# Kernel tuning notes

Measured on AMD Instinct MI355X. Metric: run time of the kernel, lower is better.

## Reference

```python
import jax, jax.numpy as jnp
import numpy as np

B, N, D = 8, 2048, 512   # batch, ctx_size, input_size
P, H = 16, 32            # num_pers, hidden_size


def setup_inputs() -> dict:
    key = jax.random.key(0)
    k1, k2 = jax.random.split(key)
    context = jax.random.normal(k1, (B, N, D), dtype=jnp.float32)
    # stacked weights of the 16 bias-free nn.Linear(input_size, hidden_size) layers
    # xavier-uniform-style scale: sqrt(6/(fan_in+fan_out))
    limit = np.sqrt(6.0 / (D + H)).astype(np.float32)
    W = jax.random.uniform(k2, (P, H, D), dtype=jnp.float32, minval=-limit, maxval=limit)
    ctx_mask = jnp.ones((B, N), dtype=jnp.int32)
    return {"context": context, "W": W, "ctx_mask": ctx_mask}


def reference(context, W, ctx_mask):
    # per-persona projection + relu: [P, B, N, H]
    fc = jax.nn.relu(jnp.einsum('bnd,phd->pbnh', context, W))
    # sum over personas of fc @ fc^T, then average: [B, N, N]
    att = jnp.einsum('pbnh,pbmh->bnm', fc, fc) / P
    # NOTE: original uses F.softmax(attention, dim=1) -> softmax over rows (axis=1)
    att = jax.nn.softmax(att, axis=1)
    # masked_fill with markoff_value=0 on masked columns then masked rows
    m = ctx_mask.astype(att.dtype)          # [B, N]
    att = att * m[:, None, :] * m[:, :, None]
    return att
```

## Files before the change

### kernel.cpp

```cpp
#include <hip/hip_runtime.h>

#define Bc 8
#define Nc 2048
#define Dc 512
#define PH 512
#define NN 4194304
#define NT 136

#define BM 128
#define BN 128
#define BK 32

typedef __attribute__((ext_vector_type(8))) short bf16x8;
typedef __attribute__((ext_vector_type(4))) float f32x4;

static __device__ __forceinline__ unsigned short f2b(float x) {
    union { float f; unsigned u; } v; v.f = x;
    unsigned r = v.u + 0x7fffu + ((v.u >> 16) & 1u);
    return (unsigned short)(r >> 16);
}

static __device__ __forceinline__ void load16_lds(const unsigned short* g, unsigned short* l) {
    __builtin_amdgcn_global_load_lds(
        (const __attribute__((address_space(1))) void*)g,
        (__attribute__((address_space(3))) void*)l,
        16, 0, 0);
}

__global__ __launch_bounds__(256) void prep_kernel(
    const float* __restrict__ ctx, const float* __restrict__ W,
    unsigned short* __restrict__ Xb, unsigned short* __restrict__ Wb,
    float* __restrict__ rsum) {
    int t = blockIdx.x * 256 + threadIdx.x;
    if (t < 2097152) {
        float4 v = ((const float4*)ctx)[t];
        ushort4 o;
        o.x = f2b(v.x); o.y = f2b(v.y); o.z = f2b(v.z); o.w = f2b(v.w);
        ((ushort4*)Xb)[t] = o;
    }
    if (t < 65536) {
        float4 v = ((const float4*)W)[t];
        ushort4 o;
        o.x = f2b(v.x); o.y = f2b(v.y); o.z = f2b(v.z); o.w = f2b(v.w);
        ((ushort4*)Wb)[t] = o;
    }
    if (t < 4096) {
        float4 z; z.x = 0.f; z.y = 0.f; z.z = 0.f; z.w = 0.f;
        ((float4*)rsum)[t] = z;
    }
}

__global__ __launch_bounds__(256) void gemm1_relu(
    const unsigned short* __restrict__ Xb, const unsigned short* __restrict__ Wb,
    unsigned short* __restrict__ F) {
    __shared__ unsigned short As[BM * BK];
    __shared__ unsigned short Bs[BN * BK];
    const int tid = threadIdx.x;
    const int lane = tid & 63;
    const int wave = tid >> 6;
    const int wm = wave >> 1, wn = wave & 1;
    const int row0 = blockIdx.y * BM;
    const int col0 = blockIdx.x * BN;

    f32x4 acc[4][4] = {};

    for (int k0 = 0; k0 < Dc; k0 += BK) {
#pragma unroll
        for (int j = 0; j < 2; ++j) {
            int e = j * 256 + tid;
            int rr = e >> 2, cc = e & 3;
            load16_lds(&Xb[(size_t)(row0 + rr) * Dc + k0 + cc * 8], &As[e * 8]);
            load16_lds(&Wb[(size_t)(col0 + rr) * Dc + k0 + cc * 8], &Bs[e * 8]);
        }
        __syncthreads();

        bf16x8 af[4], bfr[4];
#pragma unroll
        for (int i = 0; i < 4; ++i) {
            af[i]  = *(const bf16x8*)&As[(wm * 64 + i * 16 + (lane & 15)) * BK + (lane >> 4) * 8];
            bfr[i] = *(const bf16x8*)&Bs[(wn * 64 + i * 16 + (lane & 15)) * BK + (lane >> 4) * 8];
        }
#pragma unroll
        for (int mi = 0; mi < 4; ++mi)
#pragma unroll
            for (int ni = 0; ni < 4; ++ni)
                acc[mi][ni] = __builtin_amdgcn_mfma_f32_16x16x32_bf16(af[mi], bfr[ni], acc[mi][ni], 0, 0, 0);
        __syncthreads();
    }

#pragma unroll
    for (int mi = 0; mi < 4; ++mi) {
#pragma unroll
        for (int ni = 0; ni < 4; ++ni) {
            int col  = col0 + wn * 64 + ni * 16 + (lane & 15);
            int rowb = row0 + wm * 64 + mi * 16 + ((lane >> 4) << 2);
#pragma unroll
            for (int r = 0; r < 4; ++r) {
                float v = fmaxf(acc[mi][ni][r], 0.0f);
                F[(size_t)(rowb + r) * PH + col] = f2b(v);
            }
        }
    }
}

__global__ __launch_bounds__(256) void gemm2_store(
    const unsigned short* __restrict__ F, float* __restrict__ rsum,
    float* __restrict__ Ework) {
    __shared__ unsigned short As[BM * BK];
    __shared__ unsigned short Bs[BN * BK];
    const int tid = threadIdx.x;
    const int lane = tid & 63;
    const int wave = tid >> 6;
    const int wm = wave >> 1, wn = wave & 1;
    const int l15 = lane & 15, q = lane >> 4;
    const int b = blockIdx.x & 7;
    const int idx = blockIdx.x >> 3;

    int j = 0;
    while (((j + 1) * (j + 2) / 2) <= idx) ++j;
    int i = idx - j * (j + 1) / 2;
    const int row0 = i * BM;
    const int col0 = j * BN;
    const unsigned short* Fb = F + (size_t)b * Nc * PH;

    f32x4 acc[4][4] = {};

    for (int k0 = 0; k0 < PH; k0 += BK) {
#pragma unroll
        for (int jj = 0; jj < 2; ++jj) {
            int e = jj * 256 + tid;
            int rr = e >> 2, cc = e & 3;
            load16_lds(&Fb[(size_t)(row0 + rr) * PH + k0 + cc * 8], &As[e * 8]);
            load16_lds(&Fb[(size_t)(col0 + rr) * PH + k0 + cc * 8], &Bs[e * 8]);
        }
        __syncthreads();

        bf16x8 af[4], bfr[4];
#pragma unroll
        for (int qq = 0; qq < 4; ++qq) {
            af[qq]  = *(const bf16x8*)&As[(wm * 64 + qq * 16 + l15) * BK + q * 8];
            bfr[qq] = *(const bf16x8*)&Bs[(wn * 64 + qq * 16 + l15) * BK + q * 8];
        }
#pragma unroll
        for (int mi = 0; mi < 4; ++mi)
#pragma unroll
            for (int ni = 0; ni < 4; ++ni)
                acc[mi][ni] = __builtin_amdgcn_mfma_f32_16x16x32_bf16(af[mi], bfr[ni], acc[mi][ni], 0, 0, 0);
        __syncthreads();
    }

    float* Et = Ework + (size_t)(b * NT + idx) * 16384;

    float csum[4] = {0.f, 0.f, 0.f, 0.f};
    float rsm[4][4];
#pragma unroll
    for (int mi = 0; mi < 4; ++mi)
#pragma unroll
        for (int r = 0; r < 4; ++r) rsm[mi][r] = 0.f;

#pragma unroll
    for (int mi = 0; mi < 4; ++mi) {
#pragma unroll
        for (int ni = 0; ni < 4; ++ni) {
#pragma unroll
            for (int r = 0; r < 4; ++r) {
                float e = __expf(acc[mi][ni][r] * 0.0625f - 32.0f);
                Et[(wm * 64 + mi * 16 + (q << 2) + r) * 128 + wn * 64 + ni * 16 + l15] = e;
                csum[ni] += e;
                rsm[mi][r] += e;
            }
        }
    }
#pragma unroll
    for (int ni = 0; ni < 4; ++ni) {
        float s = csum[ni];
        s += __shfl_xor(s, 16);
        s += __shfl_xor(s, 32);
        if ((lane >> 4) == 0)
            atomicAdd(&rsum[b * Nc + col0 + wn * 64 + ni * 16 + lane], s);
    }
    if (i != j) {
#pragma unroll
        for (int mi = 0; mi < 4; ++mi) {
#pragma unroll
            for (int r = 0; r < 4; ++r) {
                float s = rsm[mi][r];
                s += __shfl_xor(s, 1);
                s += __shfl_xor(s, 2);
                s += __shfl_xor(s, 4);
                s += __shfl_xor(s, 8);
                if ((lane & 15) == 0)
                    atomicAdd(&rsum[b * Nc + row0 + wm * 64 + mi * 16 + ((lane >> 4) << 2) + r], s);
            }
        }
    }
}

__global__ __launch_bounds__(256) void invr_kernel(
    const float* __restrict__ rsum, const int* __restrict__ mask,
    float* __restrict__ invr) {
    int t = blockIdx.x * 256 + threadIdx.x;
    if (t < Bc * Nc) invr[t] = (float)mask[t] / rsum[t];
}

__global__ __launch_bounds__(256) void scatter_out(
    const float* __restrict__ Ework, const float* __restrict__ invr,
    const int* __restrict__ mask, float* __restrict__ out) {
    __shared__ float Ts[32 * 132];
    const int tid = threadIdx.x;
    const int b = blockIdx.x & 7;
    const int idx = blockIdx.x >> 3;

    int j = 0;
    while (((j + 1) * (j + 2) / 2) <= idx) ++j;
    int i = idx - j * (j + 1) / 2;
    const int row0 = i * BM;
    const int col0 = j * BN;

    const float* Et   = Ework + (size_t)(b * NT + idx) * 16384;
    const float* invb = invr + b * Nc;
    const int*   mb   = mask + b * Nc;
    float* outb = out + (size_t)b * NN;

    const int cl = tid >> 3, f0 = tid & 7;
    const int mc = tid >> 1, h  = tid & 1;

    for (int ci = 0; ci < 4; ++ci) {
        if (ci) __syncthreads();
        const int r = ci * 32 + cl;
        const int n = row0 + r;
        const float mrow = (float)mb[n];
#pragma unroll
        for (int g = 0; g < 4; ++g) {
            int f = f0 + 8 * g;
            float4 ev = *(const float4*)&Et[r * 128 + 4 * f];
            *(float4*)&Ts[cl * 132 + 4 * f] = ev;
            float4 iv = *(const float4*)&invb[col0 + 4 * f];
            float4 o;
            o.x = ev.x * iv.x * mrow;
            o.y = ev.y * iv.y * mrow;
            o.z = ev.z * iv.z * mrow;
            o.w = ev.w * iv.w * mrow;
            *(float4*)&outb[(size_t)n * Nc + col0 + 4 * f] = o;
        }
        if (i == j) continue;
        __syncthreads();
        const int a = col0 + mc;
        const float mcol = (float)mb[a];
        const int nb0 = row0 + ci * 32 + 16 * h;
#pragma unroll
        for (int u = 0; u < 4; ++u) {
            float4 iv = *(const float4*)&invb[nb0 + 4 * u];
            float4 o;
            o.x = Ts[(16 * h + 4 * u + 0) * 132 + mc] * iv.x * mcol;
            o.y = Ts[(16 * h + 4 * u + 1) * 132 + mc] * iv.y * mcol;
            o.z = Ts[(16 * h + 4 * u + 2) * 132 + mc] * iv.z * mcol;
            o.w = Ts[(16 * h + 4 * u + 3) * 132 + mc] * iv.w * mcol;
            *(float4*)&outb[(size_t)a * Nc + nb0 + 4 * u] = o;
        }
    }
}

__global__ __launch_bounds__(256) void gemm2_rsum(
    const unsigned short* __restrict__ F, float* __restrict__ rsum) {
    __shared__ unsigned short As[BM * BK];
    __shared__ unsigned short Bs[BN * BK];
    const int tid = threadIdx.x;
    const int lane = tid & 63;
    const int wave = tid >> 6;
    const int wm = wave >> 1, wn = wave & 1;
    const int b = blockIdx.y;

    int idx = blockIdx.x;
    int j = 0;
    while (((j + 1) * (j + 2) / 2) <= idx) ++j;
    int i = idx - j * (j + 1) / 2;
    const int row0 = i * BM;
    const int col0 = j * BN;
    const unsigned short* Fb = F + (size_t)b * Nc * PH;

    f32x4 acc[4][4] = {};

    for (int k0 = 0; k0 < PH; k0 += BK) {
#pragma unroll
        for (int jj = 0; jj < 2; ++jj) {
            int e = jj * 256 + tid;
            int rr = e >> 2, cc = e & 3;
            load16_lds(&Fb[(size_t)(row0 + rr) * PH + k0 + cc * 8], &As[e * 8]);
            load16_lds(&Fb[(size_t)(col0 + rr) * PH + k0 + cc * 8], &Bs[e * 8]);
        }
        __syncthreads();

        bf16x8 af[4], bfr[4];
#pragma unroll
        for (int q = 0; q < 4; ++q) {
            af[q]  = *(const bf16x8*)&As[(wm * 64 + q * 16 + (lane & 15)) * BK + (lane >> 4) * 8];
            bfr[q] = *(const bf16x8*)&Bs[(wn * 64 + q * 16 + (lane & 15)) * BK + (lane >> 4) * 8];
        }
#pragma unroll
        for (int mi = 0; mi < 4; ++mi)
#pragma unroll
            for (int ni = 0; ni < 4; ++ni)
                acc[mi][ni] = __builtin_amdgcn_mfma_f32_16x16x32_bf16(af[mi], bfr[ni], acc[mi][ni], 0, 0, 0);
        __syncthreads();
    }

    float csum[4] = {0.f, 0.f, 0.f, 0.f};
    float rsm[4][4];
#pragma unroll
    for (int mi = 0; mi < 4; ++mi)
#pragma unroll
        for (int r = 0; r < 4; ++r) rsm[mi][r] = 0.f;

#pragma unroll
    for (int mi = 0; mi < 4; ++mi) {
#pragma unroll
        for (int ni = 0; ni < 4; ++ni) {
#pragma unroll
            for (int r = 0; r < 4; ++r) {
                float e = __expf(acc[mi][ni][r] * 0.0625f - 32.0f);
                csum[ni] += e;
                rsm[mi][r] += e;
            }
        }
    }
#pragma unroll
    for (int ni = 0; ni < 4; ++ni) {
        float s = csum[ni];
        s += __shfl_xor(s, 16);
        s += __shfl_xor(s, 32);
        if ((lane >> 4) == 0)
            atomicAdd(&rsum[b * Nc + col0 + wn * 64 + ni * 16 + lane], s);
    }
    if (i != j) {
#pragma unroll
        for (int mi = 0; mi < 4; ++mi) {
#pragma unroll
            for (int r = 0; r < 4; ++r) {
                float s = rsm[mi][r];
                s += __shfl_xor(s, 1);
                s += __shfl_xor(s, 2);
                s += __shfl_xor(s, 4);
                s += __shfl_xor(s, 8);
                if ((lane & 15) == 0)
                    atomicAdd(&rsum[b * Nc + row0 + wm * 64 + mi * 16 + ((lane >> 4) << 2) + r], s);
            }
        }
    }
}

__global__ __launch_bounds__(256) void gemm2_write_sym(
    const unsigned short* __restrict__ F, const float* __restrict__ invr,
    const int* __restrict__ mask, float* __restrict__ out) {
    __shared__ unsigned short As[BM * BK];
    __shared__ unsigned short Bs[BN * BK];
    __shared__ float Ts[32 * 132];
    const int tid = threadIdx.x;
    const int lane = tid & 63;
    const int wave = tid >> 6;
    const int wm = wave >> 1, wn = wave & 1;
    const int l15 = lane & 15, q = lane >> 4;
    const int b = blockIdx.y;

    int idx = blockIdx.x;
    int j = 0;
    while (((j + 1) * (j + 2) / 2) <= idx) ++j;
    int i = idx - j * (j + 1) / 2;
    const int row0 = i * BM;
    const int col0 = j * BN;
    const unsigned short* Fb = F + (size_t)b * Nc * PH;

    f32x4 acc[4][4] = {};

    for (int k0 = 0; k0 < PH; k0 += BK) {
#pragma unroll
        for (int jj = 0; jj < 2; ++jj) {
            int e = jj * 256 + tid;
            int rr = e >> 2, cc = e & 3;
            load16_lds(&Fb[(size_t)(row0 + rr) * PH + k0 + cc * 8], &As[e * 8]);
            load16_lds(&Fb[(size_t)(col0 + rr) * PH + k0 + cc * 8], &Bs[e * 8]);
        }
        __syncthreads();

        bf16x8 af[4], bfr[4];
#pragma unroll
        for (int qq = 0; qq < 4; ++qq) {
            af[qq]  = *(const bf16x8*)&As[(wm * 64 + qq * 16 + l15) * BK + q * 8];
            bfr[qq] = *(const bf16x8*)&Bs[(wn * 64 + qq * 16 + l15) * BK + q * 8];
        }
#pragma unroll
        for (int mi = 0; mi < 4; ++mi)
#pragma unroll
            for (int ni = 0; ni < 4; ++ni)
                acc[mi][ni] = __builtin_amdgcn_mfma_f32_16x16x32_bf16(af[mi], bfr[ni], acc[mi][ni], 0, 0, 0);
        __syncthreads();
    }

#pragma unroll
    for (int mi = 0; mi < 4; ++mi)
#pragma unroll
        for (int ni = 0; ni < 4; ++ni)
#pragma unroll
            for (int r = 0; r < 4; ++r)
                acc[mi][ni][r] = __expf(acc[mi][ni][r] * 0.0625f - 32.0f);

    float* outb = out + (size_t)b * NN;

    float iv[4];
#pragma unroll
    for (int ni = 0; ni < 4; ++ni)
        iv[ni] = invr[b * Nc + col0 + wn * 64 + ni * 16 + l15];
#pragma unroll
    for (int mi = 0; mi < 4; ++mi) {
        int rowb = row0 + wm * 64 + mi * 16 + (q << 2);
        const int4 mr4 = *(const int4*)&mask[b * Nc + rowb];
        float mr[4] = {(float)mr4.x, (float)mr4.y, (float)mr4.z, (float)mr4.w};
#pragma unroll
        for (int ni = 0; ni < 4; ++ni) {
            int col = col0 + wn * 64 + ni * 16 + l15;
#pragma unroll
            for (int r = 0; r < 4; ++r)
                outb[(size_t)(rowb + r) * Nc + col] = acc[mi][ni][r] * iv[ni] * mr[r];
        }
    }

    if (i != j) {
#pragma unroll
        for (int ci = 0; ci < 4; ++ci) {
            __syncthreads();
            if (wn == (ci >> 1)) {
#pragma unroll
                for (int ni2 = 0; ni2 < 2; ++ni2) {
                    int ni = (ci & 1) * 2 + ni2;
#pragma unroll
                    for (int mi = 0; mi < 4; ++mi) {
                        *(float4*)&Ts[(ni2 * 16 + l15) * 132 + wm * 64 + mi * 16 + (q << 2)] =
                            *(float4*)&acc[mi][ni];
                    }
                }
            }
            __syncthreads();
            int cl = tid >> 3;
            int f0 = tid & 7;
            int nn = col0 + ci * 32 + cl;
            float mrow = (float)mask[b * Nc + nn];
            float* orow = &outb[(size_t)nn * Nc + row0];
#pragma unroll
            for (int g = 0; g < 4; ++g) {
                int f = f0 + g * 8;
                float4 ev  = *(float4*)&Ts[cl * 132 + 4 * f];
                float4 iv4 = *(const float4*)&invr[b * Nc + row0 + 4 * f];
                float4 o;
                o.x = ev.x * iv4.x * mrow;
                o.y = ev.y * iv4.y * mrow;
                o.z = ev.z * iv4.z * mrow;
                o.w = ev.w * iv4.w * mrow;
                *(float4*)&orow[4 * f] = o;
            }
        }
    }
}

extern "C" void kernel_launch(void* const* d_in, const int* in_sizes, int n_in,
                              void* d_out, int out_size, void* d_ws, size_t ws_size,
                              hipStream_t stream) {
    const float* ctx  = (const float*)d_in[0];
    const float* W    = (const float*)d_in[1];
    const int*   mask = (const int*)d_in[2];
    float* out = (float*)d_out;

    char* ws = (char*)d_ws;

    const size_t NEED = 88211456;

    if (ws_size >= NEED) {
        float*          Ework = (float*)ws;
        unsigned short* Xb    = (unsigned short*)ws;
        unsigned short* Wb    = (unsigned short*)(ws + 16777216);
        unsigned short* F     = (unsigned short*)(ws + 71303168);
        float*          rsum  = (float*)(ws + 88080384);
        float*          invr  = (float*)(ws + 88145920);

        prep_kernel<<<8192, 256, 0, stream>>>(ctx, W, Xb, Wb, rsum);
        gemm1_relu<<<dim3(4, 128), 256, 0, stream>>>(Xb, Wb, F);
        gemm2_store<<<1088, 256, 0, stream>>>(F, rsum, Ework);
        invr_kernel<<<64, 256, 0, stream>>>(rsum, mask, invr);
        scatter_out<<<1088, 256, 0, stream>>>(Ework, invr, mask, out);
    } else {
        unsigned short* Xb = (unsigned short*)ws;
        unsigned short* Wb = (unsigned short*)(ws + 16777216);
        unsigned short* F  = (unsigned short*)(ws + 16777216 + 524288);
        float* rsum        = (float*)(ws + 16777216 + 524288 + 16777216);
        float* invr        = (float*)(ws + 16777216 + 524288 + 16777216 + 65536);

        prep_kernel<<<8192, 256, 0, stream>>>(ctx, W, Xb, Wb, rsum);
        gemm1_relu<<<dim3(4, 128), 256, 0, stream>>>(Xb, Wb, F);
        gemm2_rsum<<<dim3(136, 8), 256, 0, stream>>>(F, rsum);
        invr_kernel<<<64, 256, 0, stream>>>(rsum, mask, invr);
        gemm2_write_sym<<<dim3(136, 8), 256, 0, stream>>>(F, invr, mask, out);
    }
}
```

Before: 236.0 us.

## Replace GEMM kernels with 256x256-tile 8-phase pipelined MFMA kernels

Replaces both the projection GEMM and the symmetric Gram GEMM with 512-thread, 256x256-tile kernels. They use 128KB of dynamic LDS with double-buffered, XOR-swizzled K-halves, and an 8-phase schedule that interleaves global->LDS loads with MFMA bursts under setprio and explicit waitcnt/barriers. The Gram kernel still writes per-128-block exp tiles so the existing scatter stage is unchanged. The larger tiles are meant to cut LDS/global traffic per flop and hide load latency. The costs are far fewer blocks (128 and 288), which may underfill 256 CUs, and a fragile hand-tuned waitcnt scheme.

```diff
diff --git a/kernel.cpp b/kernel.cpp
--- a/kernel.cpp
+++ b/kernel.cpp
@@ -47,6 +47,251 @@
     if (t < 4096) {
         float4 z; z.x = 0.f; z.y = 0.f; z.z = 0.f; z.w = 0.f;
         ((float4*)rsum)[t] = z;
+    }
+}
+
+#define SLOT_U(par, kh, isA) ((((par)*2 + (kh))*2 + (isA)) * 8192)
+
+#define STAGE_HALF(isA_, kh_, par_, ktv) do {                                   \
+    int ktm_ = (ktv) & 7;                                                       \
+    const unsigned short* g_ = (isA_) ? (Aop) : (Bop);                          \
+    int r0_ = (isA_) ? (arow0) : (bcol0);                                       \
+    unsigned short* lb_ = &Ls[SLOT_U(par_, kh_, isA_)];                         \
+    _Pragma("unroll")                                                           \
+    for (int l_ = 0; l_ < 2; ++l_) {                                            \
+        int d_  = (l_*512 + tid) * 16;                                          \
+        int dz_ = d_ ^ (((d_>>9)&1)<<5);                                        \
+        load16_lds(&g_[(size_t)(r0_ + (dz_>>6)) * 512 + ktm_*64 + (kh_)*32 + ((dz_&63)>>1)], \
+                   &lb_[d_>>1]);                                                \
+    }                                                                           \
+} while (0)
+
+#define PHASE(Q_, KS_, PAR_, SA_, SKH_, SPAR_, SKT_, DOVM_) do {                \
+    if ((Q_) == 0) {                                                            \
+        bq0 = *(const bf16x8*)&Ls[SLOT_U(PAR_, KS_, 0) + boff + 0*512];         \
+        bq1 = *(const bf16x8*)&Ls[SLOT_U(PAR_, KS_, 0) + boff + 1*512];         \
+        bq2 = *(const bf16x8*)&Ls[SLOT_U(PAR_, KS_, 0) + boff + 2*512];         \
+        bq3 = *(const bf16x8*)&Ls[SLOT_U(PAR_, KS_, 0) + boff + 3*512];         \
+    }                                                                           \
+    bf16x8 a0_ = *(const bf16x8*)&Ls[SLOT_U(PAR_, KS_, 1) + aoff + ((Q_)*4+0)*512]; \
+    bf16x8 a1_ = *(const bf16x8*)&Ls[SLOT_U(PAR_, KS_, 1) + aoff + ((Q_)*4+1)*512]; \
+    bf16x8 a2_ = *(const bf16x8*)&Ls[SLOT_U(PAR_, KS_, 1) + aoff + ((Q_)*4+2)*512]; \
+    bf16x8 a3_ = *(const bf16x8*)&Ls[SLOT_U(PAR_, KS_, 1) + aoff + ((Q_)*4+3)*512]; \
+    STAGE_HALF(SA_, SKH_, SPAR_, SKT_);                                         \
+    __builtin_amdgcn_s_barrier();                                               \
+    asm volatile("s_waitcnt lgkmcnt(0)" ::: "memory");                          \
+    __builtin_amdgcn_sched_barrier(0);                                          \
+    __builtin_amdgcn_s_setprio(1);                                              \
+    acc[(Q_)*4+0][0] = __builtin_amdgcn_mfma_f32_16x16x32_bf16(a0_, bq0, acc[(Q_)*4+0][0], 0, 0, 0); \
+    acc[(Q_)*4+0][1] = __builtin_amdgcn_mfma_f32_16x16x32_bf16(a0_, bq1, acc[(Q_)*4+0][1], 0, 0, 0); \
+    acc[(Q_)*4+0][2] = __builtin_amdgcn_mfma_f32_16x16x32_bf16(a0_, bq2, acc[(Q_)*4+0][2], 0, 0, 0); \
+    acc[(Q_)*4+0][3] = __builtin_amdgcn_mfma_f32_16x16x32_bf16(a0_, bq3, acc[(Q_)*4+0][3], 0, 0, 0); \
+    acc[(Q_)*4+1][0] = __builtin_amdgcn_mfma_f32_16x16x32_bf16(a1_, bq0, acc[(Q_)*4+1][0], 0, 0, 0); \
+    acc[(Q_)*4+1][1] = __builtin_amdgcn_mfma_f32_16x16x32_bf16(a1_, bq1, acc[(Q_)*4+1][1], 0, 0, 0); \
+    acc[(Q_)*4+1][2] = __builtin_amdgcn_mfma_f32_16x16x32_bf16(a1_, bq2, acc[(Q_)*4+1][2], 0, 0, 0); \
+    acc[(Q_)*4+1][3] = __builtin_amdgcn_mfma_f32_16x16x32_bf16(a1_, bq3, acc[(Q_)*4+1][3], 0, 0, 0); \
+    acc[(Q_)*4+2][0] = __builtin_amdgcn_mfma_f32_16x16x32_bf16(a2_, bq0, acc[(Q_)*4+2][0], 0, 0, 0); \
+    acc[(Q_)*4+2][1] = __builtin_amdgcn_mfma_f32_16x16x32_bf16(a2_, bq1, acc[(Q_)*4+2][1], 0, 0, 0); \
+    acc[(Q_)*4+2][2] = __builtin_amdgcn_mfma_f32_16x16x32_bf16(a2_, bq2, acc[(Q_)*4+2][2], 0, 0, 0); \
+    acc[(Q_)*4+2][3] = __builtin_amdgcn_mfma_f32_16x16x32_bf16(a2_, bq3, acc[(Q_)*4+2][3], 0, 0, 0); \
+    acc[(Q_)*4+3][0] = __builtin_amdgcn_mfma_f32_16x16x32_bf16(a3_, bq0, acc[(Q_)*4+3][0], 0, 0, 0); \
+    acc[(Q_)*4+3][1] = __builtin_amdgcn_mfma_f32_16x16x32_bf16(a3_, bq1, acc[(Q_)*4+3][1], 0, 0, 0); \
+    acc[(Q_)*4+3][2] = __builtin_amdgcn_mfma_f32_16x16x32_bf16(a3_, bq2, acc[(Q_)*4+3][2], 0, 0, 0); \
+    acc[(Q_)*4+3][3] = __builtin_amdgcn_mfma_f32_16x16x32_bf16(a3_, bq3, acc[(Q_)*4+3][3], 0, 0, 0); \
+    __builtin_amdgcn_s_setprio(0);                                              \
+    if (DOVM_) { asm volatile("s_waitcnt vmcnt(6)" ::: "memory"); }             \
+    __builtin_amdgcn_s_barrier();                                               \
+} while (0)
+
+#define GEMM256_CORE() do {                                                     \
+    STAGE_HALF(0,0,0, 0); STAGE_HALF(1,0,0, 0); STAGE_HALF(0,1,0, 0); STAGE_HALF(1,1,0, 0); \
+    STAGE_HALF(0,0,1, 1); STAGE_HALF(1,0,1, 1); STAGE_HALF(0,1,1, 1);           \
+    asm volatile("s_waitcnt vmcnt(6)" ::: "memory");                            \
+    __builtin_amdgcn_s_barrier();                                               \
+    for (int it = 0; it < 4; ++it) {                                            \
+        const int k1 = 2*it + 1, k2 = 2*it + 2, k3 = 2*it + 3;                  \
+        PHASE(0,0,0,  1,1,1, k1, 0);                                            \
+        PHASE(1,0,0,  0,0,0, k2, 0);                                            \
+        PHASE(0,1,0,  1,0,0, k2, 0);                                            \
+        PHASE(1,1,0,  0,1,0, k2, 1);                                            \
+        PHASE(0,0,1,  1,1,0, k2, 0);                                            \
+        PHASE(1,0,1,  0,0,1, k3, 0);                                            \
+        PHASE(0,1,1,  1,0,1, k3, 0);                                            \
+        PHASE(1,1,1,  0,1,1, k3, 1);                                            \
+    }                                                                           \
+} while (0)
+
+#define GEMM256_IDS()                                                           \
+    const int tid = threadIdx.x;                                                \
+    const int lane = tid & 63;                                                  \
+    const int wv = tid >> 6;                                                    \
+    const int wm = wv >> 2, wn = wv & 3;                                        \
+    const int l15 = lane & 15, q4 = lane >> 4;                                  \
+    const int sxu = ((l15 >> 3) & 1) << 4;                                      \
+    const int aoff = ((((wm*128 + l15) << 5) + (q4 << 3)) ^ sxu);               \
+    const int boff = ((((wn*64  + l15) << 5) + (q4 << 3)) ^ sxu);
+
+__global__ __launch_bounds__(512, 2) void gemm1_8ph(
+    const unsigned short* __restrict__ Xb, const unsigned short* __restrict__ Wb,
+    unsigned short* __restrict__ F) {
+    extern __shared__ __align__(16) unsigned short Ls[];
+    GEMM256_IDS();
+    const int I = blockIdx.x >> 1, Jn = blockIdx.x & 1;
+    const unsigned short* Aop = Xb;
+    const unsigned short* Bop = Wb;
+    const int arow0 = I * 256, bcol0 = Jn * 256;
+
+    f32x4 acc[8][4] = {};
+    bf16x8 bq0, bq1, bq2, bq3;
+    GEMM256_CORE();
+
+#pragma unroll
+    for (int fi = 0; fi < 8; ++fi) {
+        const int row = I*256 + wm*128 + fi*16 + q4*4;
+#pragma unroll
+        for (int ni = 0; ni < 4; ++ni) {
+            const int col = Jn*256 + wn*64 + ni*16 + l15;
+#pragma unroll
+            for (int r = 0; r < 4; ++r)
+                F[(size_t)(row + r) * PH + col] = f2b(fmaxf(acc[fi][ni][r], 0.0f));
+        }
+    }
+}
+
+__global__ __launch_bounds__(512, 2) void gemm2_store_8ph(
+    const unsigned short* __restrict__ Fm, float* __restrict__ rsum,
+    float* __restrict__ Ework) {
+    extern __shared__ __align__(16) unsigned short Ls[];
+    GEMM256_IDS();
+    const int b = blockIdx.x & 7;
+    const int T = blockIdx.x >> 3;
+    int J = 0;
+    while (((J + 1) * (J + 2) / 2) <= T) ++J;
+    const int I = T - J * (J + 1) / 2;
+    const unsigned short* Fb = Fm + (size_t)b * Nc * PH;
+    const unsigned short* Aop = Fb;
+    const unsigned short* Bop = Fb;
+    const int arow0 = I * 256, bcol0 = J * 256;
+
+    f32x4 acc[8][4] = {};
+    bf16x8 bq0, bq1, bq2, bq3;
+    GEMM256_CORE();
+
+    const int sj = wn >> 1;
+    const int i128 = 2*I + wm, j128 = 2*J + sj;
+    if (!(I == J && wm == 1 && sj == 0)) {
+        const int idx128 = j128 * (j128 + 1) / 2 + i128;
+        float* Et = Ework + (size_t)(b * NT + idx128) * 16384;
+        const int colb = (wn & 1) * 64;
+
+        float csum[4] = {0.f, 0.f, 0.f, 0.f};
+        float rsm[8][4];
+#pragma unroll
+        for (int fi = 0; fi < 8; ++fi)
+#pragma unroll
+            for (int r = 0; r < 4; ++r) rsm[fi][r] = 0.f;
+
+#pragma unroll
+        for (int fi = 0; fi < 8; ++fi) {
+#pragma unroll
+            for (int ni = 0; ni < 4; ++ni) {
+#pragma unroll
+                for (int r = 0; r < 4; ++r) {
+                    float e = __expf(acc[fi][ni][r] * 0.0625f - 32.0f);
+                    Et[(fi*16 + q4*4 + r) * 128 + colb + ni*16 + l15] = e;
+                    csum[ni] += e;
+                    rsm[fi][r] += e;
+                }
+            }
+        }
+#pragma unroll
+        for (int ni = 0; ni < 4; ++ni) {
+            float s = csum[ni];
+            s += __shfl_xor(s, 16);
+            s += __shfl_xor(s, 32);
+            if (q4 == 0)
+                atomicAdd(&rsum[b*Nc + J*256 + wn*64 + ni*16 + l15], s);
+        }
+        if (i128 != j128) {
+#pragma unroll
+            for (int fi = 0; fi < 8; ++fi) {
+#pragma unroll
+                for (int r = 0; r < 4; ++r) {
+                    float s = rsm[fi][r];
+                    s += __shfl_xor(s, 1);
+                    s += __shfl_xor(s, 2);
+                    s += __shfl_xor(s, 4);
+                    s += __shfl_xor(s, 8);
+                    if (l15 == 0)
+                        atomicAdd(&rsum[b*Nc + I*256 + wm*128 + fi*16 + q4*4 + r], s);
+                }
+            }
+        }
+    }
+}
+
+__global__ __launch_bounds__(256) void invr_kernel(
+    const float* __restrict__ rsum, const int* __restrict__ mask,
+    float* __restrict__ invr) {
+    int t = blockIdx.x * 256 + threadIdx.x;
+    if (t < Bc * Nc) invr[t] = (float)mask[t] / rsum[t];
+}
+
+__global__ __launch_bounds__(256) void scatter_out(
+    const float* __restrict__ Ework, const float* __restrict__ invr,
+    const int* __restrict__ mask, float* __restrict__ out) {
+    __shared__ float Ts[32 * 132];
+    const int tid = threadIdx.x;
+    const int b = blockIdx.x & 7;
+    const int idx = blockIdx.x >> 3;
+
+    int j = 0;
+    while (((j + 1) * (j + 2) / 2) <= idx) ++j;
+    int i = idx - j * (j + 1) / 2;
+    const int row0 = i * BM;
+    const int col0 = j * BN;
+
+    const float* Et   = Ework + (size_t)(b * NT + idx) * 16384;
+    const float* invb = invr + b * Nc;
+    const int*   mb   = mask + b * Nc;
+    float* outb = out + (size_t)b * NN;
+
+    const int cl = tid >> 3, f0 = tid & 7;
+    const int mc = tid >> 1, h  = tid & 1;
+
+    for (int ci = 0; ci < 4; ++ci) {
+        if (ci) __syncthreads();
+        const int r = ci * 32 + cl;
+        const int n = row0 + r;
+        const float mrow = (float)mb[n];
+#pragma unroll
+        for (int g = 0; g < 4; ++g) {
+            int f = f0 + 8 * g;
+            float4 ev = *(const float4*)&Et[r * 128 + 4 * f];
+            *(float4*)&Ts[cl * 132 + 4 * f] = ev;
+            float4 iv = *(const float4*)&invb[col0 + 4 * f];
+            float4 o;
+            o.x = ev.x * iv.x * mrow;
+            o.y = ev.y * iv.y * mrow;
+            o.z = ev.z * iv.z * mrow;
+            o.w = ev.w * iv.w * mrow;
+            *(float4*)&outb[(size_t)n * Nc + col0 + 4 * f] = o;
+        }
+        if (i == j) continue;
+        __syncthreads();
+        const int a = col0 + mc;
+        const float mcol = (float)mb[a];
+        const int nb0 = row0 + ci * 32 + 16 * h;
+#pragma unroll
+        for (int u = 0; u < 4; ++u) {
+            float4 iv = *(const float4*)&invb[nb0 + 4 * u];
+            float4 o;
+            o.x = Ts[(16 * h + 4 * u + 0) * 132 + mc] * iv.x * mcol;
+            o.y = Ts[(16 * h + 4 * u + 1) * 132 + mc] * iv.y * mcol;
+            o.z = Ts[(16 * h + 4 * u + 2) * 132 + mc] * iv.z * mcol;
+            o.w = Ts[(16 * h + 4 * u + 3) * 132 + mc] * iv.w * mcol;
+            *(float4*)&outb[(size_t)a * Nc + nb0 + 4 * u] = o;
+        }
     }
 }
 
@@ -99,164 +344,6 @@
                 float v = fmaxf(acc[mi][ni][r], 0.0f);
                 F[(size_t)(rowb + r) * PH + col] = f2b(v);
             }
-        }
-    }
-}
-
-__global__ __launch_bounds__(256) void gemm2_store(
-    const unsigned short* __restrict__ F, float* __restrict__ rsum,
-    float* __restrict__ Ework) {
-    __shared__ unsigned short As[BM * BK];
-    __shared__ unsigned short Bs[BN * BK];
-    const int tid = threadIdx.x;
-    const int lane = tid & 63;
-    const int wave = tid >> 6;
-    const int wm = wave >> 1, wn = wave & 1;
-    const int l15 = lane & 15, q = lane >> 4;
-    const int b = blockIdx.x & 7;
-    const int idx = blockIdx.x >> 3;
-
-    int j = 0;
-    while (((j + 1) * (j + 2) / 2) <= idx) ++j;
-    int i = idx - j * (j + 1) / 2;
-    const int row0 = i * BM;
-    const int col0 = j * BN;
-    const unsigned short* Fb = F + (size_t)b * Nc * PH;
-
-    f32x4 acc[4][4] = {};
-
-    for (int k0 = 0; k0 < PH; k0 += BK) {
-#pragma unroll
-        for (int jj = 0; jj < 2; ++jj) {
-            int e = jj * 256 + tid;
-            int rr = e >> 2, cc = e & 3;
-            load16_lds(&Fb[(size_t)(row0 + rr) * PH + k0 + cc * 8], &As[e * 8]);
-            load16_lds(&Fb[(size_t)(col0 + rr) * PH + k0 + cc * 8], &Bs[e * 8]);
-        }
-        __syncthreads();
-
-        bf16x8 af[4], bfr[4];
-#pragma unroll
-        for (int qq = 0; qq < 4; ++qq) {
-            af[qq]  = *(const bf16x8*)&As[(wm * 64 + qq * 16 + l15) * BK + q * 8];
-            bfr[qq] = *(const bf16x8*)&Bs[(wn * 64 + qq * 16 + l15) * BK + q * 8];
-        }
-#pragma unroll
-        for (int mi = 0; mi < 4; ++mi)
-#pragma unroll
-            for (int ni = 0; ni < 4; ++ni)
-                acc[mi][ni] = __builtin_amdgcn_mfma_f32_16x16x32_bf16(af[mi], bfr[ni], acc[mi][ni], 0, 0, 0);
-        __syncthreads();
-    }
-
-    float* Et = Ework + (size_t)(b * NT + idx) * 16384;
-
-    float csum[4] = {0.f, 0.f, 0.f, 0.f};
-    float rsm[4][4];
-#pragma unroll
-    for (int mi = 0; mi < 4; ++mi)
-#pragma unroll
-        for (int r = 0; r < 4; ++r) rsm[mi][r] = 0.f;
-
-#pragma unroll
-    for (int mi = 0; mi < 4; ++mi) {
-#pragma unroll
-        for (int ni = 0; ni < 4; ++ni) {
-#pragma unroll
-            for (int r = 0; r < 4; ++r) {
-                float e = __expf(acc[mi][ni][r] * 0.0625f - 32.0f);
-                Et[(wm * 64 + mi * 16 + (q << 2) + r) * 128 + wn * 64 + ni * 16 + l15] = e;
-                csum[ni] += e;
-                rsm[mi][r] += e;
-            }
-        }
-    }
-#pragma unroll
-    for (int ni = 0; ni < 4; ++ni) {
-        float s = csum[ni];
-        s += __shfl_xor(s, 16);
-        s += __shfl_xor(s, 32);
-        if ((lane >> 4) == 0)
-            atomicAdd(&rsum[b * Nc + col0 + wn * 64 + ni * 16 + lane], s);
-    }
-    if (i != j) {
-#pragma unroll
-        for (int mi = 0; mi < 4; ++mi) {
-#pragma unroll
-            for (int r = 0; r < 4; ++r) {
-                float s = rsm[mi][r];
-                s += __shfl_xor(s, 1);
-                s += __shfl_xor(s, 2);
-                s += __shfl_xor(s, 4);
-                s += __shfl_xor(s, 8);
-                if ((lane & 15) == 0)
-                    atomicAdd(&rsum[b * Nc + row0 + wm * 64 + mi * 16 + ((lane >> 4) << 2) + r], s);
-            }
-        }
-    }
-}
-
-__global__ __launch_bounds__(256) void invr_kernel(
-    const float* __restrict__ rsum, const int* __restrict__ mask,
-    float* __restrict__ invr) {
-    int t = blockIdx.x * 256 + threadIdx.x;
-    if (t < Bc * Nc) invr[t] = (float)mask[t] / rsum[t];
-}
-
-__global__ __launch_bounds__(256) void scatter_out(
-    const float* __restrict__ Ework, const float* __restrict__ invr,
-    const int* __restrict__ mask, float* __restrict__ out) {
-    __shared__ float Ts[32 * 132];
-    const int tid = threadIdx.x;
-    const int b = blockIdx.x & 7;
-    const int idx = blockIdx.x >> 3;
-
-    int j = 0;
-    while (((j + 1) * (j + 2) / 2) <= idx) ++j;
-    int i = idx - j * (j + 1) / 2;
-    const int row0 = i * BM;
-    const int col0 = j * BN;
-
-    const float* Et   = Ework + (size_t)(b * NT + idx) * 16384;
-    const float* invb = invr + b * Nc;
-    const int*   mb   = mask + b * Nc;
-    float* outb = out + (size_t)b * NN;
-
-    const int cl = tid >> 3, f0 = tid & 7;
-    const int mc = tid >> 1, h  = tid & 1;
-
-    for (int ci = 0; ci < 4; ++ci) {
-        if (ci) __syncthreads();
-        const int r = ci * 32 + cl;
-        const int n = row0 + r;
-        const float mrow = (float)mb[n];
-#pragma unroll
-        for (int g = 0; g < 4; ++g) {
-            int f = f0 + 8 * g;
-            float4 ev = *(const float4*)&Et[r * 128 + 4 * f];
-            *(float4*)&Ts[cl * 132 + 4 * f] = ev;
-            float4 iv = *(const float4*)&invb[col0 + 4 * f];
-            float4 o;
-            o.x = ev.x * iv.x * mrow;
-            o.y = ev.y * iv.y * mrow;
-            o.z = ev.z * iv.z * mrow;
-            o.w = ev.w * iv.w * mrow;
-            *(float4*)&outb[(size_t)n * Nc + col0 + 4 * f] = o;
-        }
-        if (i == j) continue;
-        __syncthreads();
-        const int a = col0 + mc;
-        const float mcol = (float)mb[a];
-        const int nb0 = row0 + ci * 32 + 16 * h;
-#pragma unroll
-        for (int u = 0; u < 4; ++u) {
-            float4 iv = *(const float4*)&invb[nb0 + 4 * u];
-            float4 o;
-            o.x = Ts[(16 * h + 4 * u + 0) * 132 + mc] * iv.x * mcol;
-            o.y = Ts[(16 * h + 4 * u + 1) * 132 + mc] * iv.y * mcol;
-            o.z = Ts[(16 * h + 4 * u + 2) * 132 + mc] * iv.z * mcol;
-            o.w = Ts[(16 * h + 4 * u + 3) * 132 + mc] * iv.w * mcol;
-            *(float4*)&outb[(size_t)a * Nc + nb0 + 4 * u] = o;
         }
     }
 }
@@ -481,9 +568,14 @@
         float*          rsum  = (float*)(ws + 88080384);
         float*          invr  = (float*)(ws + 88145920);
 
+        hipFuncSetAttribute(reinterpret_cast<const void*>(gemm1_8ph),
+                            hipFuncAttributeMaxDynamicSharedMemorySize, 131072);
+        hipFuncSetAttribute(reinterpret_cast<const void*>(gemm2_store_8ph),
+                            hipFuncAttributeMaxDynamicSharedMemorySize, 131072);
+
         prep_kernel<<<8192, 256, 0, stream>>>(ctx, W, Xb, Wb, rsum);
-        gemm1_relu<<<dim3(4, 128), 256, 0, stream>>>(Xb, Wb, F);
-        gemm2_store<<<1088, 256, 0, stream>>>(F, rsum, Ework);
+        gemm1_8ph<<<128, 512, 131072, stream>>>(Xb, Wb, F);
+        gemm2_store_8ph<<<288, 512, 131072, stream>>>(F, rsum, Ework);
         invr_kernel<<<64, 256, 0, stream>>>(rsum, mask, invr);
         scatter_out<<<1088, 256, 0, stream>>>(Ework, invr, mask, out);
     } else {
```

After: 251.4 us. 1.07x slower.

## Store symmetric exp tiles as fp16 using diagonal-based rescaling

Applied to the files above, without the earlier changes.

Adds a diag kernel that computes each row's self-similarity h and exp(h), then stores exp(S - h_row - h_col) as fp16 instead of fp32. The row-sum and output scaling factors are corrected with exp(h). Halving the intermediate buffer cuts the write and read traffic between the gemm2_store and scatter_out kernels and shrinks the workspace. The cost is an extra kernel pass over F and a loss of fp16 precision and range in the stored exponentials.

```diff
diff --git a/kernel.cpp b/kernel.cpp
--- a/kernel.cpp
+++ b/kernel.cpp
@@ -18,6 +18,11 @@
     union { float f; unsigned u; } v; v.f = x;
     unsigned r = v.u + 0x7fffu + ((v.u >> 16) & 1u);
     return (unsigned short)(r >> 16);
+}
+
+static __device__ __forceinline__ unsigned short f2h(float x) {
+    _Float16 h = (_Float16)x;
+    return __builtin_bit_cast(unsigned short, h);
 }
 
 static __device__ __forceinline__ void load16_lds(const unsigned short* g, unsigned short* l) {
@@ -103,9 +108,41 @@
     }
 }
 
+__global__ __launch_bounds__(256) void diag_kernel(
+    const unsigned short* __restrict__ F, float* __restrict__ hd,
+    float* __restrict__ pH) {
+    const int row = blockIdx.x * 4 + (threadIdx.x >> 6);
+    const int lane = threadIdx.x & 63;
+    uint4 u = *(const uint4*)(F + (size_t)row * PH + lane * 8);
+    float s = 0.f;
+    {
+        float a0 = __builtin_bit_cast(float, u.x << 16);
+        float a1 = __builtin_bit_cast(float, u.x & 0xffff0000u);
+        float a2 = __builtin_bit_cast(float, u.y << 16);
+        float a3 = __builtin_bit_cast(float, u.y & 0xffff0000u);
+        float a4 = __builtin_bit_cast(float, u.z << 16);
+        float a5 = __builtin_bit_cast(float, u.z & 0xffff0000u);
+        float a6 = __builtin_bit_cast(float, u.w << 16);
+        float a7 = __builtin_bit_cast(float, u.w & 0xffff0000u);
+        s = a0*a0 + a1*a1 + a2*a2 + a3*a3 + a4*a4 + a5*a5 + a6*a6 + a7*a7;
+    }
+    s += __shfl_xor(s, 1);
+    s += __shfl_xor(s, 2);
+    s += __shfl_xor(s, 4);
+    s += __shfl_xor(s, 8);
+    s += __shfl_xor(s, 16);
+    s += __shfl_xor(s, 32);
+    if (lane == 0) {
+        float h = s * 0.03125f;
+        hd[row] = h;
+        pH[row] = __expf(h);
+    }
+}
+
 __global__ __launch_bounds__(256) void gemm2_store(
-    const unsigned short* __restrict__ F, float* __restrict__ rsum,
-    float* __restrict__ Ework) {
+    const unsigned short* __restrict__ F, const float* __restrict__ hd,
+    const float* __restrict__ pH, float* __restrict__ rsum,
+    unsigned short* __restrict__ Ework) {
     __shared__ unsigned short As[BM * BK];
     __shared__ unsigned short Bs[BN * BK];
     const int tid = threadIdx.x;
@@ -149,7 +186,24 @@
         __syncthreads();
     }
 
-    float* Et = Ework + (size_t)(b * NT + idx) * 16384;
+    const float* hdb = hd + b * Nc;
+    const float* pHb = pH + b * Nc;
+    unsigned short* Et = Ework + (size_t)(b * NT + idx) * 16384;
+
+    float hcol[4], phc[4];
+#pragma unroll
+    for (int ni = 0; ni < 4; ++ni) {
+        int col = col0 + wn * 64 + ni * 16 + l15;
+        hcol[ni] = hdb[col];
+        phc[ni]  = pHb[col];
+    }
+    f32x4 hrow[4], phr[4];
+#pragma unroll
+    for (int mi = 0; mi < 4; ++mi) {
+        int rw = row0 + wm * 64 + mi * 16 + (q << 2);
+        hrow[mi] = *(const f32x4*)&hdb[rw];
+        phr[mi]  = *(const f32x4*)&pHb[rw];
+    }
 
     float csum[4] = {0.f, 0.f, 0.f, 0.f};
     float rsm[4][4];
@@ -164,10 +218,10 @@
         for (int ni = 0; ni < 4; ++ni) {
 #pragma unroll
             for (int r = 0; r < 4; ++r) {
-                float e = __expf(acc[mi][ni][r] * 0.0625f - 32.0f);
-                Et[(wm * 64 + mi * 16 + (q << 2) + r) * 128 + wn * 64 + ni * 16 + l15] = e;
-                csum[ni] += e;
-                rsm[mi][r] += e;
+                float e = __expf(acc[mi][ni][r] * 0.0625f - hcol[ni] - hrow[mi][r]);
+                Et[(wm * 64 + mi * 16 + (q << 2) + r) * 128 + wn * 64 + ni * 16 + l15] = f2h(e);
+                csum[ni] += e * phr[mi][r];
+                rsm[mi][r] += e * phc[ni];
             }
         }
     }
@@ -204,8 +258,9 @@
 }
 
 __global__ __launch_bounds__(256) void scatter_out(
-    const float* __restrict__ Ework, const float* __restrict__ invr,
-    const int* __restrict__ mask, float* __restrict__ out) {
+    const unsigned short* __restrict__ Ework, const float* __restrict__ invr,
+    const float* __restrict__ pH, const int* __restrict__ mask,
+    float* __restrict__ out) {
     __shared__ float Ts[32 * 132];
     const int tid = threadIdx.x;
     const int b = blockIdx.x & 7;
@@ -217,8 +272,9 @@
     const int row0 = i * BM;
     const int col0 = j * BN;
 
-    const float* Et   = Ework + (size_t)(b * NT + idx) * 16384;
+    const unsigned short* Et = Ework + (size_t)(b * NT + idx) * 16384;
     const float* invb = invr + b * Nc;
+    const float* pHb  = pH + b * Nc;
     const int*   mb   = mask + b * Nc;
     float* outb = out + (size_t)b * NN;
 
@@ -229,33 +285,44 @@
         if (ci) __syncthreads();
         const int r = ci * 32 + cl;
         const int n = row0 + r;
-        const float mrow = (float)mb[n];
-#pragma unroll
-        for (int g = 0; g < 4; ++g) {
-            int f = f0 + 8 * g;
-            float4 ev = *(const float4*)&Et[r * 128 + 4 * f];
-            *(float4*)&Ts[cl * 132 + 4 * f] = ev;
-            float4 iv = *(const float4*)&invb[col0 + 4 * f];
-            float4 o;
-            o.x = ev.x * iv.x * mrow;
-            o.y = ev.y * iv.y * mrow;
-            o.z = ev.z * iv.z * mrow;
-            o.w = ev.w * iv.w * mrow;
-            *(float4*)&outb[(size_t)n * Nc + col0 + 4 * f] = o;
+        const float mrow = (float)mb[n] * pHb[n];
+#pragma unroll
+        for (int g = 0; g < 2; ++g) {
+            const int c0 = 64 * g + 8 * f0;
+            union { int4 iv; _Float16 hv[8]; } u;
+            u.iv = *(const int4*)&Et[r * 128 + c0];
+            float ev[8];
+#pragma unroll
+            for (int k = 0; k < 8; ++k) ev[k] = (float)u.hv[k];
+            *(float4*)&Ts[cl * 132 + c0]     = *(float4*)&ev[0];
+            *(float4*)&Ts[cl * 132 + c0 + 4] = *(float4*)&ev[4];
+            float4 iv0 = *(const float4*)&invb[col0 + c0];
+            float4 iv1 = *(const float4*)&invb[col0 + c0 + 4];
+            float4 o0, o1;
+            o0.x = ev[0] * iv0.x * mrow;
+            o0.y = ev[1] * iv0.y * mrow;
+            o0.z = ev[2] * iv0.z * mrow;
+            o0.w = ev[3] * iv0.w * mrow;
+            o1.x = ev[4] * iv1.x * mrow;
+            o1.y = ev[5] * iv1.y * mrow;
+            o1.z = ev[6] * iv1.z * mrow;
+            o1.w = ev[7] * iv1.w * mrow;
+            *(float4*)&outb[(size_t)n * Nc + col0 + c0]     = o0;
+            *(float4*)&outb[(size_t)n * Nc + col0 + c0 + 4] = o1;
         }
         if (i == j) continue;
         __syncthreads();
         const int a = col0 + mc;
-        const float mcol = (float)mb[a];
+        const float mrowB = (float)mb[a] * pHb[a];
         const int nb0 = row0 + ci * 32 + 16 * h;
 #pragma unroll
         for (int u = 0; u < 4; ++u) {
             float4 iv = *(const float4*)&invb[nb0 + 4 * u];
             float4 o;
-            o.x = Ts[(16 * h + 4 * u + 0) * 132 + mc] * iv.x * mcol;
-            o.y = Ts[(16 * h + 4 * u + 1) * 132 + mc] * iv.y * mcol;
-            o.z = Ts[(16 * h + 4 * u + 2) * 132 + mc] * iv.z * mcol;
-            o.w = Ts[(16 * h + 4 * u + 3) * 132 + mc] * iv.w * mcol;
+            o.x = Ts[(16 * h + 4 * u + 0) * 132 + mc] * iv.x * mrowB;
+            o.y = Ts[(16 * h + 4 * u + 1) * 132 + mc] * iv.y * mrowB;
+            o.z = Ts[(16 * h + 4 * u + 2) * 132 + mc] * iv.z * mrowB;
+            o.w = Ts[(16 * h + 4 * u + 3) * 132 + mc] * iv.w * mrowB;
             *(float4*)&outb[(size_t)a * Nc + nb0 + 4 * u] = o;
         }
     }
@@ -471,21 +538,24 @@
 
     char* ws = (char*)d_ws;
 
-    const size_t NEED = 88211456;
+    const size_t NEED = 52690944;
 
     if (ws_size >= NEED) {
-        float*          Ework = (float*)ws;
+        unsigned short* Ework = (unsigned short*)ws;
         unsigned short* Xb    = (unsigned short*)ws;
         unsigned short* Wb    = (unsigned short*)(ws + 16777216);
-        unsigned short* F     = (unsigned short*)(ws + 71303168);
-        float*          rsum  = (float*)(ws + 88080384);
-        float*          invr  = (float*)(ws + 88145920);
+        unsigned short* F     = (unsigned short*)(ws + 35651584);
+        float*          rsum  = (float*)(ws + 52428800);
+        float*          invr  = (float*)(ws + 52494336);
+        float*          hd    = (float*)(ws + 52559872);
+        float*          pH    = (float*)(ws + 52625408);
 
         prep_kernel<<<8192, 256, 0, stream>>>(ctx, W, Xb, Wb, rsum);
         gemm1_relu<<<dim3(4, 128), 256, 0, stream>>>(Xb, Wb, F);
-        gemm2_store<<<1088, 256, 0, stream>>>(F, rsum, Ework);
+        diag_kernel<<<4096, 256, 0, stream>>>(F, hd, pH);
+        gemm2_store<<<1088, 256, 0, stream>>>(F, hd, pH, rsum, Ework);
         invr_kernel<<<64, 256, 0, stream>>>(rsum, mask, invr);
-        scatter_out<<<1088, 256, 0, stream>>>(Ework, invr, mask, out);
+        scatter_out<<<1088, 256, 0, stream>>>(Ework, invr, pH, mask, out);
     } else {
         unsigned short* Xb = (unsigned short*)ws;
         unsigned short* Wb = (unsigned short*)(ws + 16777216);
```

Measured after the change: 246.1 us. 1.04x slower.

## Store intermediate exp tile in bf16, fold inverse-sum into scatter, swizzle gemm1 grid

Applied to the files above, without the earlier changes.

The exp tile workspace written by gemm2_store and read by scatter_out is now stored as bf16 instead of fp32, halving that intermediate traffic. The separate invr kernel is removed from the main path, and each scatter block computes its own 128-entry row and column inverse sums into LDS. gemm1_relu is launched on a 1D grid with a swizzled block-to-tile mapping meant to improve L2 reuse, and the old 2D variant is kept as a fallback. Rounding the exp values to bf16 before normalisation reduces output precision.

```diff
diff --git a/kernel.cpp b/kernel.cpp
--- a/kernel.cpp
+++ b/kernel.cpp
@@ -18,6 +18,10 @@
     union { float f; unsigned u; } v; v.f = x;
     unsigned r = v.u + 0x7fffu + ((v.u >> 16) & 1u);
     return (unsigned short)(r >> 16);
+}
+
+static __device__ __forceinline__ float b2f(unsigned short x) {
+    return __builtin_bit_cast(float, (unsigned)x << 16);
 }
 
 static __device__ __forceinline__ void load16_lds(const unsigned short* g, unsigned short* l) {
@@ -59,8 +63,9 @@
     const int lane = tid & 63;
     const int wave = tid >> 6;
     const int wm = wave >> 1, wn = wave & 1;
-    const int row0 = blockIdx.y * BM;
-    const int col0 = blockIdx.x * BN;
+    const int bid = blockIdx.x;
+    const int row0 = ((bid & 7) + ((bid >> 5) << 3)) * BM;
+    const int col0 = ((bid >> 3) & 3) * BN;
 
     f32x4 acc[4][4] = {};
 
@@ -105,7 +110,7 @@
 
 __global__ __launch_bounds__(256) void gemm2_store(
     const unsigned short* __restrict__ F, float* __restrict__ rsum,
-    float* __restrict__ Ework) {
+    unsigned short* __restrict__ Ework) {
     __shared__ unsigned short As[BM * BK];
     __shared__ unsigned short Bs[BN * BK];
     const int tid = threadIdx.x;
@@ -149,7 +154,7 @@
         __syncthreads();
     }
 
-    float* Et = Ework + (size_t)(b * NT + idx) * 16384;
+    unsigned short* Et = Ework + (size_t)(b * NT + idx) * 16384;
 
     float csum[4] = {0.f, 0.f, 0.f, 0.f};
     float rsm[4][4];
@@ -165,7 +170,7 @@
 #pragma unroll
             for (int r = 0; r < 4; ++r) {
                 float e = __expf(acc[mi][ni][r] * 0.0625f - 32.0f);
-                Et[(wm * 64 + mi * 16 + (q << 2) + r) * 128 + wn * 64 + ni * 16 + l15] = e;
+                Et[(wm * 64 + mi * 16 + (q << 2) + r) * 128 + wn * 64 + ni * 16 + l15] = f2b(e);
                 csum[ni] += e;
                 rsm[mi][r] += e;
             }
@@ -196,17 +201,12 @@
     }
 }
 
-__global__ __launch_bounds__(256) void invr_kernel(
-    const float* __restrict__ rsum, const int* __restrict__ mask,
-    float* __restrict__ invr) {
-    int t = blockIdx.x * 256 + threadIdx.x;
-    if (t < Bc * Nc) invr[t] = (float)mask[t] / rsum[t];
-}
-
 __global__ __launch_bounds__(256) void scatter_out(
-    const float* __restrict__ Ework, const float* __restrict__ invr,
+    const unsigned short* __restrict__ Ework, const float* __restrict__ rsum,
     const int* __restrict__ mask, float* __restrict__ out) {
     __shared__ float Ts[32 * 132];
+    __shared__ float invA[128];
+    __shared__ float invB[128];
     const int tid = threadIdx.x;
     const int b = blockIdx.x & 7;
     const int idx = blockIdx.x >> 3;
@@ -217,10 +217,14 @@
     const int row0 = i * BM;
     const int col0 = j * BN;
 
-    const float* Et   = Ework + (size_t)(b * NT + idx) * 16384;
-    const float* invb = invr + b * Nc;
+    const unsigned short* Et = Ework + (size_t)(b * NT + idx) * 16384;
+    const float* rsb  = rsum + b * Nc;
     const int*   mb   = mask + b * Nc;
     float* outb = out + (size_t)b * NN;
+
+    if (tid < 128)       invA[tid]       = (float)mb[col0 + tid]       / rsb[col0 + tid];
+    else                 invB[tid - 128] = (float)mb[row0 + tid - 128] / rsb[row0 + tid - 128];
+    __syncthreads();
 
     const int cl = tid >> 3, f0 = tid & 7;
     const int mc = tid >> 1, h  = tid & 1;
@@ -231,32 +235,104 @@
         const int n = row0 + r;
         const float mrow = (float)mb[n];
 #pragma unroll
-        for (int g = 0; g < 4; ++g) {
-            int f = f0 + 8 * g;
-            float4 ev = *(const float4*)&Et[r * 128 + 4 * f];
-            *(float4*)&Ts[cl * 132 + 4 * f] = ev;
-            float4 iv = *(const float4*)&invb[col0 + 4 * f];
-            float4 o;
-            o.x = ev.x * iv.x * mrow;
-            o.y = ev.y * iv.y * mrow;
-            o.z = ev.z * iv.z * mrow;
-            o.w = ev.w * iv.w * mrow;
-            *(float4*)&outb[(size_t)n * Nc + col0 + 4 * f] = o;
+        for (int g = 0; g < 2; ++g) {
+            const int c0 = 64 * g + 8 * f0;
+            union { int4 iv; unsigned short hv[8]; } u;
+            u.iv = *(const int4*)&Et[r * 128 + c0];
+            float ev[8];
+#pragma unroll
+            for (int k = 0; k < 8; ++k) ev[k] = b2f(u.hv[k]);
+            *(float4*)&Ts[cl * 132 + c0]     = *(float4*)&ev[0];
+            *(float4*)&Ts[cl * 132 + c0 + 4] = *(float4*)&ev[4];
+            float4 iv0 = *(const float4*)&invA[c0];
+            float4 iv1 = *(const float4*)&invA[c0 + 4];
+            float4 o0, o1;
+            o0.x = ev[0] * iv0.x * mrow;
+            o0.y = ev[1] * iv0.y * mrow;
+            o0.z = ev[2] * iv0.z * mrow;
+            o0.w = ev[3] * iv0.w * mrow;
+            o1.x = ev[4] * iv1.x * mrow;
+            o1.y = ev[5] * iv1.y * mrow;
+            o1.z = ev[6] * iv1.z * mrow;
+            o1.w = ev[7] * iv1.w * mrow;
+            *(float4*)&outb[(size_t)n * Nc + col0 + c0]     = o0;
+            *(float4*)&outb[(size_t)n * Nc + col0 + c0 + 4] = o1;
         }
         if (i == j) continue;
         __syncthreads();
         const int a = col0 + mc;
         const float mcol = (float)mb[a];
-        const int nb0 = row0 + ci * 32 + 16 * h;
+        const int lb0 = ci * 32 + 16 * h;
+        const int nb0 = row0 + lb0;
 #pragma unroll
         for (int u = 0; u < 4; ++u) {
-            float4 iv = *(const float4*)&invb[nb0 + 4 * u];
+            float4 iv = *(const float4*)&invB[lb0 + 4 * u];
             float4 o;
             o.x = Ts[(16 * h + 4 * u + 0) * 132 + mc] * iv.x * mcol;
             o.y = Ts[(16 * h + 4 * u + 1) * 132 + mc] * iv.y * mcol;
             o.z = Ts[(16 * h + 4 * u + 2) * 132 + mc] * iv.z * mcol;
             o.w = Ts[(16 * h + 4 * u + 3) * 132 + mc] * iv.w * mcol;
             *(float4*)&outb[(size_t)a * Nc + nb0 + 4 * u] = o;
+        }
+    }
+}
+
+__global__ __launch_bounds__(256) void invr_kernel(
+    const float* __restrict__ rsum, const int* __restrict__ mask,
+    float* __restrict__ invr) {
+    int t = blockIdx.x * 256 + threadIdx.x;
+    if (t < Bc * Nc) invr[t] = (float)mask[t] / rsum[t];
+}
+
+__global__ __launch_bounds__(256) void gemm1_relu_fb(
+    const unsigned short* __restrict__ Xb, const unsigned short* __restrict__ Wb,
+    unsigned short* __restrict__ F) {
+    __shared__ unsigned short As[BM * BK];
+    __shared__ unsigned short Bs[BN * BK];
+    const int tid = threadIdx.x;
+    const int lane = tid & 63;
+    const int wave = tid >> 6;
+    const int wm = wave >> 1, wn = wave & 1;
+    const int row0 = blockIdx.y * BM;
+    const int col0 = blockIdx.x * BN;
+
+    f32x4 acc[4][4] = {};
+
+    for (int k0 = 0; k0 < Dc; k0 += BK) {
+#pragma unroll
+        for (int j = 0; j < 2; ++j) {
+            int e = j * 256 + tid;
+            int rr = e >> 2, cc = e & 3;
+            load16_lds(&Xb[(size_t)(row0 + rr) * Dc + k0 + cc * 8], &As[e * 8]);
+            load16_lds(&Wb[(size_t)(col0 + rr) * Dc + k0 + cc * 8], &Bs[e * 8]);
+        }
+        __syncthreads();
+
+        bf16x8 af[4], bfr[4];
+#pragma unroll
+        for (int i = 0; i < 4; ++i) {
+            af[i]  = *(const bf16x8*)&As[(wm * 64 + i * 16 + (lane & 15)) * BK + (lane >> 4) * 8];
+            bfr[i] = *(const bf16x8*)&Bs[(wn * 64 + i * 16 + (lane & 15)) * BK + (lane >> 4) * 8];
+        }
+#pragma unroll
+        for (int mi = 0; mi < 4; ++mi)
+#pragma unroll
+            for (int ni = 0; ni < 4; ++ni)
+                acc[mi][ni] = __builtin_amdgcn_mfma_f32_16x16x32_bf16(af[mi], bfr[ni], acc[mi][ni], 0, 0, 0);
+        __syncthreads();
+    }
+
+#pragma unroll
+    for (int mi = 0; mi < 4; ++mi) {
+#pragma unroll
+        for (int ni = 0; ni < 4; ++ni) {
+            int col  = col0 + wn * 64 + ni * 16 + (lane & 15);
+            int rowb = row0 + wm * 64 + mi * 16 + ((lane >> 4) << 2);
+#pragma unroll
+            for (int r = 0; r < 4; ++r) {
+                float v = fmaxf(acc[mi][ni][r], 0.0f);
+                F[(size_t)(rowb + r) * PH + col] = f2b(v);
+            }
         }
     }
 }
@@ -471,21 +547,19 @@
 
     char* ws = (char*)d_ws;
 
-    const size_t NEED = 88211456;
+    const size_t NEED = 52494336;
 
     if (ws_size >= NEED) {
-        float*          Ework = (float*)ws;
+        unsigned short* Ework = (unsigned short*)ws;
         unsigned short* Xb    = (unsigned short*)ws;
         unsigned short* Wb    = (unsigned short*)(ws + 16777216);
-        unsigned short* F     = (unsigned short*)(ws + 71303168);
-        float*          rsum  = (float*)(ws + 88080384);
-        float*          invr  = (float*)(ws + 88145920);
+        unsigned short* F     = (unsigned short*)(ws + 35651584);
+        float*          rsum  = (float*)(ws + 52428800);
 
         prep_kernel<<<8192, 256, 0, stream>>>(ctx, W, Xb, Wb, rsum);
-        gemm1_relu<<<dim3(4, 128), 256, 0, stream>>>(Xb, Wb, F);
+        gemm1_relu<<<512, 256, 0, stream>>>(Xb, Wb, F);
         gemm2_store<<<1088, 256, 0, stream>>>(F, rsum, Ework);
-        invr_kernel<<<64, 256, 0, stream>>>(rsum, mask, invr);
-        scatter_out<<<1088, 256, 0, stream>>>(Ework, invr, mask, out);
+        scatter_out<<<1088, 256, 0, stream>>>(Ework, rsum, mask, out);
     } else {
         unsigned short* Xb = (unsigned short*)ws;
         unsigned short* Wb = (unsigned short*)(ws + 16777216);
@@ -494,7 +568,7 @@
         float* invr        = (float*)(ws + 16777216 + 524288 + 16777216 + 65536);
 
         prep_kernel<<<8192, 256, 0, stream>>>(ctx, W, Xb, Wb, rsum);
-        gemm1_relu<<<dim3(4, 128), 256, 0, stream>>>(Xb, Wb, F);
+        gemm1_relu_fb<<<dim3(4, 128), 256, 0, stream>>>(Xb, Wb, F);
         gemm2_rsum<<<dim3(136, 8), 256, 0, stream>>>(F, rsum);
         invr_kernel<<<64, 256, 0, stream>>>(rsum, mask, invr);
         gemm2_write_sym<<<dim3(136, 8), 256, 0, stream>>>(F, invr, mask, out);
```

Result: faster. 229.9 us (-2.6%).
